# Performance work log

Hardware: AMD Instinct MI355X
Metric: run time of the kernel (lower is better)

## Reference

```python
import jax, jax.numpy as jnp
import numpy as np

B, N, H, K = 8192, 256, 1024, 256
BETA = 0.99
TOL = 1e-4
MAX_ITER = 100

def V_fn(x, Wv):
    # x: (B,1,N) -> (B,1,1); positive-definite quadratic Lyapunov V(x) = ||x @ Wv||^2
    z = jnp.einsum('bon,nk->bok', x, Wv)
    return jnp.sum(z * z, axis=-1, keepdims=True)

def fhat_fn(x, W1, b1, W2, b2):
    # residual tanh MLP dynamics model fhat: (B,1,N) -> (B,1,N)
    h = jnp.tanh(jnp.einsum('bon,nh->boh', x, W1) + b1)
    return x + jnp.einsum('boh,hn->bon', h, W2) + b2

def dV_da(fx, a, Wv):
    # per-sample d/d(alpha) V(fx * alpha); mirrors torch.autograd.grad(Vfx, alpha)
    def v_scalar(a_s, fx_s):
        z = (fx_s * a_s) @ Wv
        return jnp.sum(z * z)
    g = jax.vmap(jax.grad(v_scalar))(a[:, 0, 0], fx[:, 0, :])
    return g[:, None, None]

def newton_F(fx, t, a, Wv):
    # newton_iter.forward: F = alpha - (V(fhatx*alpha) - target) / dV_da
    # dV_da was computed with create_graph=False in torch -> constant -> stop_gradient
    dv = jax.lax.stop_gradient(dV_da(fx, a, Wv))
    return a - (V_fn(fx * a, Wv) - t) / dv

def solve_alpha(fhatx, target, Wv):
    # vectorized Newton + bisection with per-sample masking (rootfind_train.forward)
    Bn = fhatx.shape[0]
    alpha0 = jnp.ones((Bn, 1, 1), jnp.float32)
    e1_0 = jnp.zeros_like(alpha0)
    e2_0 = jnp.ones_like(alpha0)
    m0 = (V_fn(fhatx, Wv) - target) > 0.0

    def cond(c):
        a, e1, e2, m, it = c
        return jnp.logical_and(jnp.any(m), it < MAX_ITER)

    def body(c):
        a, e1, e2, m, it = c
        a = jnp.where(m, newton_F(fhatx, target, a, Wv), a)
        m_bis = (a < e1) | (a > e2)
        a_bis = e1 + (e2 - e1) / 2
        sa = jnp.sign(V_fn(fhatx * a_bis, Wv) - target)
        s1 = jnp.sign(V_fn(fhatx * e1, Wv) - target)
        s2 = jnp.sign(V_fn(fhatx * e2, Wv) - target)
        m_end2 = m_bis & (sa * s1 < 0)
        m_end1 = m_bis & (sa * s2 < 0)
        e2 = jnp.where(m_end2, a_bis, e2)
        e1 = jnp.where(m_end1, a_bis, e1)
        a = jnp.where(m_bis, a_bis, a)
        m = jnp.abs(V_fn(fhatx * a, Wv) - target) > TOL
        return (a, e1, e2, m, it + 1)

    a, _, _, _, _ = jax.lax.while_loop(cond, body, (alpha0, e1_0, e2_0, m0, jnp.int32(0)))
    return a

def setup_inputs() -> dict:
    key = jax.random.key(0)
    ks = jax.random.split(key, 4)
    x = jax.random.normal(ks[0], (B, 1, N), jnp.float32)
    W1 = jax.random.normal(ks[1], (N, H), jnp.float32) / np.sqrt(N)
    b1 = jnp.zeros((H,), jnp.float32)
    W2 = jax.random.normal(ks[2], (H, N), jnp.float32) * (0.5 / np.sqrt(H))
    b2 = jnp.zeros((N,), jnp.float32)
    Wv = jax.random.normal(ks[3], (N, K), jnp.float32) / np.sqrt(N)
    return {'x': x, 'W1': W1, 'b1': b1, 'W2': W2, 'b2': b2, 'Wv': Wv}

def reference(x, W1, b1, W2, b2, Wv):
    fhatx = fhat_fn(x, W1, b1, W2, b2)
    target = BETA * V_fn(x, Wv)
    alpha = jax.lax.stop_gradient(solve_alpha(fhatx, target, Wv))  # alpha detached in torch
    return fhatx * alpha
```

## Files before the change

kernel.cpp:

```cpp
#include <hip/hip_runtime.h>
#include <math.h>

typedef __attribute__((ext_vector_type(8))) short bf16x8;
typedef __attribute__((ext_vector_type(4))) float f32x4;

static __device__ __forceinline__ unsigned short f2bf(float f) {
  union { float f; unsigned u; } a; a.f = f;
  unsigned u = a.u;
  unsigned r = u + 0x7FFF + ((u >> 16) & 1);
  return (unsigned short)(r >> 16);
}
static __device__ __forceinline__ float bf2f(unsigned short h) {
  union { unsigned u; float f; } a; a.u = ((unsigned)h) << 16;
  return a.f;
}
static __device__ __forceinline__ float tanh_fast(float x) {
  float ax = fabsf(x);
  float e = __expf(-2.0f * ax);
  float t = (1.0f - e) / (1.0f + e);
  t = (ax > 10.0f) ? 1.0f : t;
  return (x < 0.0f) ? -t : t;
}

__global__ __launch_bounds__(256) void k_split_all(
    const float* __restrict__ W1, const float* __restrict__ W2, const float* __restrict__ Wv,
    unsigned short* __restrict__ W1Th, unsigned short* __restrict__ W1Tl,
    unsigned short* __restrict__ W2Th, unsigned short* __restrict__ W2Tl,
    unsigned short* __restrict__ WvTh, unsigned short* __restrict__ WvTl)
{
  const int b = blockIdx.x;
  const float* W; unsigned short *Th, *Tl; int Kd, Nd, base;
  if (b < 1024)      { W = W1; Th = W1Th; Tl = W1Tl; Kd = 256;  Nd = 1024; base = 0; }
  else if (b < 2048) { W = W2; Th = W2Th; Tl = W2Tl; Kd = 1024; Nd = 256;  base = 1024; }
  else               { W = Wv; Th = WvTh; Tl = WvTl; Kd = 256;  Nd = 256;  base = 2048; }
  const int idx = (b - base) * 256 + threadIdx.x;
  const int k = idx % Kd, n = idx / Kd;
  const float w = W[(size_t)k * Nd + n];
  const unsigned short h = f2bf(w);
  Th[(size_t)n * Kd + k] = h;
  Tl[(size_t)n * Kd + k] = f2bf(w - bf2f(h));
}

__global__ __launch_bounds__(512, 4) void k_gemm1(
    const float* __restrict__ X, const unsigned short* __restrict__ BTh,
    const unsigned short* __restrict__ BTl, const float* __restrict__ bias,
    unsigned short* __restrict__ Hh, unsigned short* __restrict__ Hl)
{
  const int PIT = 40;
  __shared__ __align__(16) unsigned short As_h[128 * PIT], As_l[128 * PIT];
  __shared__ __align__(16) unsigned short Bs_h[128 * PIT], Bs_l[128 * PIT];
  const int t = threadIdx.x;
  const int n0 = blockIdx.x * 128, m0 = blockIdx.y * 128;
  const int l = t & 63, wid = t >> 6;
  const int wr = wid >> 2, wc = wid & 3;
  const int kk = (l >> 4) * 8;

  f32x4 acc[4][2] = {};

  for (int k0 = 0; k0 < 256; k0 += 32) {
#pragma unroll
    for (int i2 = 0; i2 < 2; ++i2) {
      const int fidx = t + i2 * 512;
      const int row = fidx >> 3, q = fidx & 7;
      const float4 v = *reinterpret_cast<const float4*>(&X[(size_t)(m0 + row) * 256 + k0 + q * 4]);
      unsigned short h0 = f2bf(v.x), h1 = f2bf(v.y), h2 = f2bf(v.z), h3 = f2bf(v.w);
      uint2 hp, lp;
      hp.x = (unsigned)h0 | ((unsigned)h1 << 16);
      hp.y = (unsigned)h2 | ((unsigned)h3 << 16);
      lp.x = (unsigned)f2bf(v.x - bf2f(h0)) | ((unsigned)f2bf(v.y - bf2f(h1)) << 16);
      lp.y = (unsigned)f2bf(v.z - bf2f(h2)) | ((unsigned)f2bf(v.w - bf2f(h3)) << 16);
      *reinterpret_cast<uint2*>(&As_h[row * PIT + q * 4]) = hp;
      *reinterpret_cast<uint2*>(&As_l[row * PIT + q * 4]) = lp;
    }
    {
      const int row = t >> 2, c4 = t & 3;
      *reinterpret_cast<uint4*>(&Bs_h[row * PIT + c4 * 8]) =
          *reinterpret_cast<const uint4*>(&BTh[(size_t)(n0 + row) * 256 + k0 + c4 * 8]);
      *reinterpret_cast<uint4*>(&Bs_l[row * PIT + c4 * 8]) =
          *reinterpret_cast<const uint4*>(&BTl[(size_t)(n0 + row) * 256 + k0 + c4 * 8]);
    }
    __syncthreads();

    bf16x8 ah[4], al[4], bh[2], bl[2];
#pragma unroll
    for (int i = 0; i < 4; ++i) {
      const int ar = wr * 64 + i * 16 + (l & 15);
      ah[i] = *reinterpret_cast<const bf16x8*>(&As_h[ar * PIT + kk]);
      al[i] = *reinterpret_cast<const bf16x8*>(&As_l[ar * PIT + kk]);
    }
#pragma unroll
    for (int j = 0; j < 2; ++j) {
      const int br = wc * 32 + j * 16 + (l & 15);
      bh[j] = *reinterpret_cast<const bf16x8*>(&Bs_h[br * PIT + kk]);
      bl[j] = *reinterpret_cast<const bf16x8*>(&Bs_l[br * PIT + kk]);
    }
#pragma unroll
    for (int i = 0; i < 4; ++i)
#pragma unroll
      for (int j = 0; j < 2; ++j) {
        acc[i][j] = __builtin_amdgcn_mfma_f32_16x16x32_bf16(ah[i], bh[j], acc[i][j], 0, 0, 0);
        acc[i][j] = __builtin_amdgcn_mfma_f32_16x16x32_bf16(ah[i], bl[j], acc[i][j], 0, 0, 0);
        acc[i][j] = __builtin_amdgcn_mfma_f32_16x16x32_bf16(al[i], bh[j], acc[i][j], 0, 0, 0);
      }
    __syncthreads();
  }

#pragma unroll
  for (int i = 0; i < 4; ++i)
#pragma unroll
    for (int j = 0; j < 2; ++j) {
      const int gn = n0 + wc * 32 + j * 16 + (l & 15);
      const float bv = bias[gn];
#pragma unroll
      for (int r = 0; r < 4; ++r) {
        const int gm = m0 + wr * 64 + i * 16 + (l >> 4) * 4 + r;
        const float tv = tanh_fast(acc[i][j][r] + bv);
        const unsigned short th = f2bf(tv);
        Hh[(size_t)gm * 1024 + gn] = th;
        Hl[(size_t)gm * 1024 + gn] = f2bf(tv - bf2f(th));
      }
    }
}

__global__ __launch_bounds__(512, 4) void k_gemm2(
    const unsigned short* __restrict__ Ah, const unsigned short* __restrict__ Al,
    const unsigned short* __restrict__ BTh, const unsigned short* __restrict__ BTl,
    const float* __restrict__ bias, const float* __restrict__ X,
    float* __restrict__ OUT)
{
  const int PIT = 72;
  __shared__ __align__(16) unsigned short As_h[64 * PIT], As_l[64 * PIT];
  __shared__ __align__(16) unsigned short Bs_h[64 * PIT], Bs_l[64 * PIT];
  const int t = threadIdx.x;
  const int n0 = blockIdx.x * 64, m0 = blockIdx.y * 64;
  const int l = t & 63, wid = t >> 6;
  const int wr = wid >> 2, wc = wid & 3;
  const int kk = (l >> 4) * 8;
  const int srow = t >> 3, c8 = t & 7;

  f32x4 acc[2] = {};

  for (int k0 = 0; k0 < 1024; k0 += 64) {
    *reinterpret_cast<uint4*>(&As_h[srow * PIT + c8 * 8]) =
        *reinterpret_cast<const uint4*>(&Ah[(size_t)(m0 + srow) * 1024 + k0 + c8 * 8]);
    *reinterpret_cast<uint4*>(&As_l[srow * PIT + c8 * 8]) =
        *reinterpret_cast<const uint4*>(&Al[(size_t)(m0 + srow) * 1024 + k0 + c8 * 8]);
    *reinterpret_cast<uint4*>(&Bs_h[srow * PIT + c8 * 8]) =
        *reinterpret_cast<const uint4*>(&BTh[(size_t)(n0 + srow) * 1024 + k0 + c8 * 8]);
    *reinterpret_cast<uint4*>(&Bs_l[srow * PIT + c8 * 8]) =
        *reinterpret_cast<const uint4*>(&BTl[(size_t)(n0 + srow) * 1024 + k0 + c8 * 8]);
    __syncthreads();

#pragma unroll
    for (int ks = 0; ks < 2; ++ks) {
      bf16x8 ah[2], al[2], bh, bl;
      const int ko = ks * 32 + kk;
#pragma unroll
      for (int i = 0; i < 2; ++i) {
        const int ar = wr * 32 + i * 16 + (l & 15);
        ah[i] = *reinterpret_cast<const bf16x8*>(&As_h[ar * PIT + ko]);
        al[i] = *reinterpret_cast<const bf16x8*>(&As_l[ar * PIT + ko]);
      }
      const int br = wc * 16 + (l & 15);
      bh = *reinterpret_cast<const bf16x8*>(&Bs_h[br * PIT + ko]);
      bl = *reinterpret_cast<const bf16x8*>(&Bs_l[br * PIT + ko]);
#pragma unroll
      for (int i = 0; i < 2; ++i) {
        acc[i] = __builtin_amdgcn_mfma_f32_16x16x32_bf16(ah[i], bh, acc[i], 0, 0, 0);
        acc[i] = __builtin_amdgcn_mfma_f32_16x16x32_bf16(ah[i], bl, acc[i], 0, 0, 0);
        acc[i] = __builtin_amdgcn_mfma_f32_16x16x32_bf16(al[i], bh, acc[i], 0, 0, 0);
      }
    }
    __syncthreads();
  }

  const int gn = n0 + wc * 16 + (l & 15);
  const float bv = bias[gn];
#pragma unroll
  for (int i = 0; i < 2; ++i)
#pragma unroll
    for (int r = 0; r < 4; ++r) {
      const int gm = m0 + wr * 32 + i * 16 + (l >> 4) * 4 + r;
      OUT[(size_t)gm * 256 + gn] = acc[i][r] + bv + X[(size_t)gm * 256 + gn];
    }
}

__global__ __launch_bounds__(512) void k_valpha(
    const float* __restrict__ X,
    const unsigned short* __restrict__ WvTh, const unsigned short* __restrict__ WvTl,
    float* __restrict__ F)
{
  __shared__ __align__(16) unsigned short Ash[32 * 256];
  __shared__ __align__(16) unsigned short Asl[32 * 256];
  __shared__ float part[2][16][8];
  __shared__ float als[16];
  const int t = threadIdx.x;
  const int l = t & 63, w = t >> 6;
  const int c = l & 15, g = l >> 4;
  const int nb = w * 32;

  bf16x8 bh[2][8], bl[2][8];
#pragma unroll
  for (int nf = 0; nf < 2; ++nf)
#pragma unroll
    for (int ks = 0; ks < 8; ++ks) {
      const int col = nb + nf * 16 + c;
      const int kof = ks * 32 + g * 8;
      bh[nf][ks] = *reinterpret_cast<const bf16x8*>(&WvTh[(size_t)col * 256 + kof]);
      bl[nf][ks] = *reinterpret_cast<const bf16x8*>(&WvTl[(size_t)col * 256 + kof]);
    }

  const int srow = t >> 4;
  const int q = t & 15;
  const int r0 = blockIdx.x * 16;

  float4 fv[4];
  {
    const float* src = (srow < 16) ? &X[(size_t)(r0 + srow) * 256]
                                   : &F[(size_t)(r0 + srow - 16) * 256];
#pragma unroll
    for (int i = 0; i < 4; ++i) {
      const float4 v = *reinterpret_cast<const float4*>(&src[q * 16 + i * 4]);
      fv[i] = v;
      const unsigned short h0 = f2bf(v.x), h1 = f2bf(v.y), h2 = f2bf(v.z), h3 = f2bf(v.w);
      uint2 hp, lp;
      hp.x = (unsigned)h0 | ((unsigned)h1 << 16);
      hp.y = (unsigned)h2 | ((unsigned)h3 << 16);
      lp.x = (unsigned)f2bf(v.x - bf2f(h0)) | ((unsigned)f2bf(v.y - bf2f(h1)) << 16);
      lp.y = (unsigned)f2bf(v.z - bf2f(h2)) | ((unsigned)f2bf(v.w - bf2f(h3)) << 16);
      const unsigned byte = (unsigned)(srow * 512 + q * 32 + i * 8) ^ ((srow & 7) << 4);
      *reinterpret_cast<uint2*>(((char*)Ash) + byte) = hp;
      *reinterpret_cast<uint2*>(((char*)Asl) + byte) = lp;
    }
  }
  __syncthreads();

  float vs[2][4] = {};
#pragma unroll
  for (int nf = 0; nf < 2; ++nf) {
    f32x4 acc0 = {}, acc1 = {};
#pragma unroll
    for (int ks = 0; ks < 8; ++ks) {
      const int kof = ks * 32 + g * 8;
      const unsigned ab0 = (unsigned)(c * 512 + kof * 2) ^ ((c & 7) << 4);
      const unsigned ab1 = (unsigned)((c + 16) * 512 + kof * 2) ^ ((c & 7) << 4);
      const bf16x8 a0h = *reinterpret_cast<const bf16x8*>(((char*)Ash) + ab0);
      const bf16x8 a0l = *reinterpret_cast<const bf16x8*>(((char*)Asl) + ab0);
      const bf16x8 a1h = *reinterpret_cast<const bf16x8*>(((char*)Ash) + ab1);
      const bf16x8 a1l = *reinterpret_cast<const bf16x8*>(((char*)Asl) + ab1);
      acc0 = __builtin_amdgcn_mfma_f32_16x16x32_bf16(a0h, bh[nf][ks], acc0, 0, 0, 0);
      acc0 = __builtin_amdgcn_mfma_f32_16x16x32_bf16(a0h, bl[nf][ks], acc0, 0, 0, 0);
      acc0 = __builtin_amdgcn_mfma_f32_16x16x32_bf16(a0l, bh[nf][ks], acc0, 0, 0, 0);
      acc1 = __builtin_amdgcn_mfma_f32_16x16x32_bf16(a1h, bh[nf][ks], acc1, 0, 0, 0);
      acc1 = __builtin_amdgcn_mfma_f32_16x16x32_bf16(a1h, bl[nf][ks], acc1, 0, 0, 0);
      acc1 = __builtin_amdgcn_mfma_f32_16x16x32_bf16(a1l, bh[nf][ks], acc1, 0, 0, 0);
    }
#pragma unroll
    for (int r = 0; r < 4; ++r) {
      vs[0][r] = fmaf(acc0[r], acc0[r], vs[0][r]);
      vs[1][r] = fmaf(acc1[r], acc1[r], vs[1][r]);
    }
  }

#pragma unroll
  for (int s = 0; s < 2; ++s)
#pragma unroll
    for (int r = 0; r < 4; ++r) {
      float v = vs[s][r];
      v += __shfl_xor(v, 1);
      v += __shfl_xor(v, 2);
      v += __shfl_xor(v, 4);
      v += __shfl_xor(v, 8);
      vs[s][r] = v;
    }
  if (c == 0) {
#pragma unroll
    for (int r = 0; r < 4; ++r) {
      part[0][g * 4 + r][w] = vs[0][r];
      part[1][g * 4 + r][w] = vs[1][r];
    }
  }
  __syncthreads();

  if (t < 16) {
    float Vx = 0.f, Vf = 0.f;
#pragma unroll
    for (int i = 0; i < 8; ++i) { Vx += part[0][t][i]; Vf += part[1][t][i]; }
    const float tt2 = 0.99f * Vx;
    float a;
    if (Vf - tt2 > 0.0f)         a = sqrtf(tt2 / Vf);
    else if (tt2 - Vf > 1e-4f)   a = 0.5f;
    else                         a = 1.0f;
    als[t] = a;
  }
  __syncthreads();

  if (srow >= 16) {
    const int row = srow - 16;
    const float a = als[row];
    float* dst = &F[(size_t)(r0 + row) * 256];
#pragma unroll
    for (int i = 0; i < 4; ++i) {
      float4 v = fv[i];
      v.x *= a; v.y *= a; v.z *= a; v.w *= a;
      *reinterpret_cast<float4*>(&dst[q * 16 + i * 4]) = v;
    }
  }
}

extern "C" void kernel_launch(void* const* d_in, const int* in_sizes, int n_in,
                              void* d_out, int out_size, void* d_ws, size_t ws_size,
                              hipStream_t stream) {
  const float* x  = (const float*)d_in[0];
  const float* W1 = (const float*)d_in[1];
  const float* b1 = (const float*)d_in[2];
  const float* W2 = (const float*)d_in[3];
  const float* b2 = (const float*)d_in[4];
  const float* Wv = (const float*)d_in[5];
  float* out = (float*)d_out;

  char* ws = (char*)d_ws;
  unsigned short* Hh   = (unsigned short*)(ws);
  unsigned short* Hl   = (unsigned short*)(ws + 16777216);
  unsigned short* W1Th = (unsigned short*)(ws + 33554432);
  unsigned short* W1Tl = (unsigned short*)(ws + 33554432 + 524288);
  unsigned short* W2Th = (unsigned short*)(ws + 33554432 + 2 * 524288);
  unsigned short* W2Tl = (unsigned short*)(ws + 33554432 + 3 * 524288);
  unsigned short* WvTh = (unsigned short*)(ws + 33554432 + 4 * 524288);
  unsigned short* WvTl = (unsigned short*)(ws + 33554432 + 4 * 524288 + 131072);

  k_split_all<<<dim3(2304), dim3(256), 0, stream>>>(W1, W2, Wv, W1Th, W1Tl, W2Th, W2Tl, WvTh, WvTl);

  k_gemm1 <<<dim3(1024 / 128, 8192 / 128), dim3(512), 0, stream>>>(x, W1Th, W1Tl, b1, Hh, Hl);
  k_gemm2 <<<dim3(256 / 64, 8192 / 64), dim3(512), 0, stream>>>(Hh, Hl, W2Th, W2Tl, b2, x, out);
  k_valpha<<<dim3(512), dim3(512), 0, stream>>>(x, WvTh, WvTl, out);
}
```

Measured before the change: 82.41 us.

## Use direct global-to-LDS loads with swizzled layout and retile both GEMMs

Pre-splits X into bf16 hi/lo planes in the prep kernel, which now also transposes the weights through shared memory with coalesced accesses. Both GEMMs load tiles with global_load_lds DMA into XOR-swizzled LDS instead of staging through registers. They also move to 256-thread blocks with larger per-wave tiles (4x4 and 2x4 MFMA fragments) to get more register reuse. The cost is extra workspace traffic for Xh/Xl, and the larger accumulators may reduce occupancy.

```diff
diff --git a/kernel.cpp b/kernel.cpp
--- a/kernel.cpp
+++ b/kernel.cpp
@@ -22,82 +22,110 @@
   return (x < 0.0f) ? -t : t;
 }
 
+static __device__ __forceinline__ void gload16(const void* g, void* l) {
+  __builtin_amdgcn_global_load_lds(
+      (const __attribute__((address_space(1))) unsigned int*)g,
+      (__attribute__((address_space(3))) unsigned int*)l, 16, 0, 0);
+}
+
 __global__ __launch_bounds__(256) void k_split_all(
-    const float* __restrict__ W1, const float* __restrict__ W2, const float* __restrict__ Wv,
+    const float* __restrict__ W1, const float* __restrict__ W2,
+    const float* __restrict__ Wv, const float* __restrict__ X,
     unsigned short* __restrict__ W1Th, unsigned short* __restrict__ W1Tl,
     unsigned short* __restrict__ W2Th, unsigned short* __restrict__ W2Tl,
-    unsigned short* __restrict__ WvTh, unsigned short* __restrict__ WvTl)
+    unsigned short* __restrict__ WvTh, unsigned short* __restrict__ WvTl,
+    unsigned short* __restrict__ Xh,  unsigned short* __restrict__ Xl)
 {
-  const int b = blockIdx.x;
-  const float* W; unsigned short *Th, *Tl; int Kd, Nd, base;
-  if (b < 1024)      { W = W1; Th = W1Th; Tl = W1Tl; Kd = 256;  Nd = 1024; base = 0; }
-  else if (b < 2048) { W = W2; Th = W2Th; Tl = W2Tl; Kd = 1024; Nd = 256;  base = 1024; }
-  else               { W = Wv; Th = WvTh; Tl = WvTl; Kd = 256;  Nd = 256;  base = 2048; }
-  const int idx = (b - base) * 256 + threadIdx.x;
-  const int k = idx % Kd, n = idx / Kd;
-  const float w = W[(size_t)k * Nd + n];
-  const unsigned short h = f2bf(w);
-  Th[(size_t)n * Kd + k] = h;
-  Tl[(size_t)n * Kd + k] = f2bf(w - bf2f(h));
-}
-
-__global__ __launch_bounds__(512, 4) void k_gemm1(
-    const float* __restrict__ X, const unsigned short* __restrict__ BTh,
-    const unsigned short* __restrict__ BTl, const float* __restrict__ bias,
+  const int b = blockIdx.x, t = threadIdx.x;
+  if (b >= 144) {
+    const size_t i0 = (size_t)(b - 144) * 2048 + (size_t)t * 8;
+    const float4 v0 = *reinterpret_cast<const float4*>(&X[i0]);
+    const float4 v1 = *reinterpret_cast<const float4*>(&X[i0 + 4]);
+    const float vv[8] = {v0.x, v0.y, v0.z, v0.w, v1.x, v1.y, v1.z, v1.w};
+    uint4 hp, lp;
+    unsigned hw[4], lw[4];
+#pragma unroll
+    for (int e = 0; e < 4; ++e) {
+      const unsigned short h0 = f2bf(vv[2*e]), h1 = f2bf(vv[2*e+1]);
+      hw[e] = (unsigned)h0 | ((unsigned)h1 << 16);
+      lw[e] = (unsigned)f2bf(vv[2*e] - bf2f(h0)) |
+              ((unsigned)f2bf(vv[2*e+1] - bf2f(h1)) << 16);
+    }
+    hp.x = hw[0]; hp.y = hw[1]; hp.z = hw[2]; hp.w = hw[3];
+    lp.x = lw[0]; lp.y = lw[1]; lp.z = lw[2]; lp.w = lw[3];
+    *reinterpret_cast<uint4*>(&Xh[i0]) = hp;
+    *reinterpret_cast<uint4*>(&Xl[i0]) = lp;
+    return;
+  }
+
+  __shared__ unsigned short shh[64 * 72], shl[64 * 72];
+  const float* W; unsigned short *Th, *Tl; int Kd, Nd, k0, n0;
+  if (b < 64)       { W = W1; Th = W1Th; Tl = W1Tl; Kd = 256;  Nd = 1024; k0 = (b & 3) * 64;        n0 = (b >> 2) * 64; }
+  else if (b < 128) { W = W2; Th = W2Th; Tl = W2Tl; Kd = 1024; Nd = 256;  k0 = ((b - 64) & 15) * 64; n0 = ((b - 64) >> 4) * 64; }
+  else              { W = Wv; Th = WvTh; Tl = WvTl; Kd = 256;  Nd = 256;  k0 = ((b - 128) & 3) * 64; n0 = ((b - 128) >> 2) * 64; }
+
+  const int kloc = t >> 4, n4 = t & 15;
+#pragma unroll
+  for (int p = 0; p < 4; ++p) {
+    const int kk = p * 16 + kloc;
+    const float4 v = *reinterpret_cast<const float4*>(&W[(size_t)(k0 + kk) * Nd + n0 + n4 * 4]);
+    const float vv[4] = {v.x, v.y, v.z, v.w};
+#pragma unroll
+    for (int e = 0; e < 4; ++e) {
+      const unsigned short hh = f2bf(vv[e]);
+      shh[(n4 * 4 + e) * 72 + kk] = hh;
+      shl[(n4 * 4 + e) * 72 + kk] = f2bf(vv[e] - bf2f(hh));
+    }
+  }
+  __syncthreads();
+  const int nl = t >> 2, ko = (t & 3) * 16;
+  const size_t dst = (size_t)(n0 + nl) * Kd + k0 + ko;
+  *reinterpret_cast<uint4*>(&Th[dst])     = *reinterpret_cast<const uint4*>(&shh[nl * 72 + ko]);
+  *reinterpret_cast<uint4*>(&Th[dst + 8]) = *reinterpret_cast<const uint4*>(&shh[nl * 72 + ko + 8]);
+  *reinterpret_cast<uint4*>(&Tl[dst])     = *reinterpret_cast<const uint4*>(&shl[nl * 72 + ko]);
+  *reinterpret_cast<uint4*>(&Tl[dst + 8]) = *reinterpret_cast<const uint4*>(&shl[nl * 72 + ko + 8]);
+}
+
+__global__ __launch_bounds__(256, 2) void k_gemm1(
+    const unsigned short* __restrict__ Xh, const unsigned short* __restrict__ Xl,
+    const unsigned short* __restrict__ BTh, const unsigned short* __restrict__ BTl,
+    const float* __restrict__ bias,
     unsigned short* __restrict__ Hh, unsigned short* __restrict__ Hl)
 {
-  const int PIT = 40;
-  __shared__ __align__(16) unsigned short As_h[128 * PIT], As_l[128 * PIT];
-  __shared__ __align__(16) unsigned short Bs_h[128 * PIT], Bs_l[128 * PIT];
-  const int t = threadIdx.x;
+  __shared__ unsigned short lds[16384];
+  const int t = threadIdx.x, l = t & 63, wv = t >> 6;
   const int n0 = blockIdx.x * 128, m0 = blockIdx.y * 128;
-  const int l = t & 63, wid = t >> 6;
-  const int wr = wid >> 2, wc = wid & 3;
-  const int kk = (l >> 4) * 8;
-
-  f32x4 acc[4][2] = {};
-
+  const int wr = wv >> 1, wc = wv & 1;
+
+  const unsigned short* ssrc = (wv == 0) ? Xh : (wv == 1) ? Xl : (wv == 2) ? BTh : BTl;
+  const int rbase = (wv < 2) ? m0 : n0;
+  char* ldsb = (char*)lds + wv * 8192;
+  const int srow = l >> 2;
+  const int sg = (l & 3) ^ ((l >> 3) & 3);
+
+  const int gofs = ((l >> 4) ^ ((l >> 1) & 3)) << 4;
+  const int arow = wr * 64 + (l & 15), brow = wc * 64 + (l & 15);
+
+  f32x4 acc[4][4] = {};
   for (int k0 = 0; k0 < 256; k0 += 32) {
 #pragma unroll
-    for (int i2 = 0; i2 < 2; ++i2) {
-      const int fidx = t + i2 * 512;
-      const int row = fidx >> 3, q = fidx & 7;
-      const float4 v = *reinterpret_cast<const float4*>(&X[(size_t)(m0 + row) * 256 + k0 + q * 4]);
-      unsigned short h0 = f2bf(v.x), h1 = f2bf(v.y), h2 = f2bf(v.z), h3 = f2bf(v.w);
-      uint2 hp, lp;
-      hp.x = (unsigned)h0 | ((unsigned)h1 << 16);
-      hp.y = (unsigned)h2 | ((unsigned)h3 << 16);
-      lp.x = (unsigned)f2bf(v.x - bf2f(h0)) | ((unsigned)f2bf(v.y - bf2f(h1)) << 16);
-      lp.y = (unsigned)f2bf(v.z - bf2f(h2)) | ((unsigned)f2bf(v.w - bf2f(h3)) << 16);
-      *reinterpret_cast<uint2*>(&As_h[row * PIT + q * 4]) = hp;
-      *reinterpret_cast<uint2*>(&As_l[row * PIT + q * 4]) = lp;
-    }
-    {
-      const int row = t >> 2, c4 = t & 3;
-      *reinterpret_cast<uint4*>(&Bs_h[row * PIT + c4 * 8]) =
-          *reinterpret_cast<const uint4*>(&BTh[(size_t)(n0 + row) * 256 + k0 + c4 * 8]);
-      *reinterpret_cast<uint4*>(&Bs_l[row * PIT + c4 * 8]) =
-          *reinterpret_cast<const uint4*>(&BTl[(size_t)(n0 + row) * 256 + k0 + c4 * 8]);
-    }
+    for (int c = 0; c < 8; ++c)
+      gload16(ssrc + (size_t)(rbase + c * 16 + srow) * 256 + k0 + sg * 8, ldsb + c * 1024);
     __syncthreads();
 
-    bf16x8 ah[4], al[4], bh[2], bl[2];
+    const char* L = (const char*)lds;
+    bf16x8 ah[4], al[4], bh[4], bl[4];
 #pragma unroll
     for (int i = 0; i < 4; ++i) {
-      const int ar = wr * 64 + i * 16 + (l & 15);
-      ah[i] = *reinterpret_cast<const bf16x8*>(&As_h[ar * PIT + kk]);
-      al[i] = *reinterpret_cast<const bf16x8*>(&As_l[ar * PIT + kk]);
-    }
-#pragma unroll
-    for (int j = 0; j < 2; ++j) {
-      const int br = wc * 32 + j * 16 + (l & 15);
-      bh[j] = *reinterpret_cast<const bf16x8*>(&Bs_h[br * PIT + kk]);
-      bl[j] = *reinterpret_cast<const bf16x8*>(&Bs_l[br * PIT + kk]);
+      ah[i] = *reinterpret_cast<const bf16x8*>(L +         (arow + i * 16) * 64 + gofs);
+      al[i] = *reinterpret_cast<const bf16x8*>(L +  8192 + (arow + i * 16) * 64 + gofs);
+      bh[i] = *reinterpret_cast<const bf16x8*>(L + 16384 + (brow + i * 16) * 64 + gofs);
+      bl[i] = *reinterpret_cast<const bf16x8*>(L + 24576 + (brow + i * 16) * 64 + gofs);
     }
 #pragma unroll
     for (int i = 0; i < 4; ++i)
 #pragma unroll
-      for (int j = 0; j < 2; ++j) {
+      for (int j = 0; j < 4; ++j) {
         acc[i][j] = __builtin_amdgcn_mfma_f32_16x16x32_bf16(ah[i], bh[j], acc[i][j], 0, 0, 0);
         acc[i][j] = __builtin_amdgcn_mfma_f32_16x16x32_bf16(ah[i], bl[j], acc[i][j], 0, 0, 0);
         acc[i][j] = __builtin_amdgcn_mfma_f32_16x16x32_bf16(al[i], bh[j], acc[i][j], 0, 0, 0);
@@ -108,8 +136,8 @@
 #pragma unroll
   for (int i = 0; i < 4; ++i)
 #pragma unroll
-    for (int j = 0; j < 2; ++j) {
-      const int gn = n0 + wc * 32 + j * 16 + (l & 15);
+    for (int j = 0; j < 4; ++j) {
+      const int gn = n0 + wc * 64 + j * 16 + (l & 15);
       const float bv = bias[gn];
 #pragma unroll
       for (int r = 0; r < 4; ++r) {
@@ -122,66 +150,72 @@
     }
 }
 
-__global__ __launch_bounds__(512, 4) void k_gemm2(
-    const unsigned short* __restrict__ Ah, const unsigned short* __restrict__ Al,
+__global__ __launch_bounds__(256, 2) void k_gemm2(
+    const unsigned short* __restrict__ Ahg, const unsigned short* __restrict__ Alg,
     const unsigned short* __restrict__ BTh, const unsigned short* __restrict__ BTl,
     const float* __restrict__ bias, const float* __restrict__ X,
     float* __restrict__ OUT)
 {
-  const int PIT = 72;
-  __shared__ __align__(16) unsigned short As_h[64 * PIT], As_l[64 * PIT];
-  __shared__ __align__(16) unsigned short Bs_h[64 * PIT], Bs_l[64 * PIT];
-  const int t = threadIdx.x;
-  const int n0 = blockIdx.x * 64, m0 = blockIdx.y * 64;
-  const int l = t & 63, wid = t >> 6;
-  const int wr = wid >> 2, wc = wid & 3;
-  const int kk = (l >> 4) * 8;
-  const int srow = t >> 3, c8 = t & 7;
-
-  f32x4 acc[2] = {};
-
+  __shared__ unsigned short lds[24576];
+  const int t = threadIdx.x, l = t & 63, wv = t >> 6;
+  const int n0 = blockIdx.x * 128, m0 = blockIdx.y * 64;
+  const int wr = wv >> 1, wc = wv & 1;
+  const int srow8 = l >> 3, sg = (l & 7) ^ (l >> 3);
+
+  f32x4 acc[2][4] = {};
   for (int k0 = 0; k0 < 1024; k0 += 64) {
-    *reinterpret_cast<uint4*>(&As_h[srow * PIT + c8 * 8]) =
-        *reinterpret_cast<const uint4*>(&Ah[(size_t)(m0 + srow) * 1024 + k0 + c8 * 8]);
-    *reinterpret_cast<uint4*>(&As_l[srow * PIT + c8 * 8]) =
-        *reinterpret_cast<const uint4*>(&Al[(size_t)(m0 + srow) * 1024 + k0 + c8 * 8]);
-    *reinterpret_cast<uint4*>(&Bs_h[srow * PIT + c8 * 8]) =
-        *reinterpret_cast<const uint4*>(&BTh[(size_t)(n0 + srow) * 1024 + k0 + c8 * 8]);
-    *reinterpret_cast<uint4*>(&Bs_l[srow * PIT + c8 * 8]) =
-        *reinterpret_cast<const uint4*>(&BTl[(size_t)(n0 + srow) * 1024 + k0 + c8 * 8]);
+#pragma unroll
+    for (int s = 0; s < 12; ++s) {
+      const int cid = wv * 12 + s;
+      const unsigned short* src; int rbase, ca, cbyte;
+      if (cid < 8)       { src = Ahg; rbase = m0; ca = cid;      cbyte = ca * 1024; }
+      else if (cid < 16) { src = Alg; rbase = m0; ca = cid - 8;  cbyte = 8192 + ca * 1024; }
+      else if (cid < 32) { src = BTh; rbase = n0; ca = cid - 16; cbyte = 16384 + ca * 1024; }
+      else               { src = BTl; rbase = n0; ca = cid - 32; cbyte = 32768 + ca * 1024; }
+      gload16(src + (size_t)(rbase + ca * 8 + srow8) * 1024 + k0 + sg * 8, (char*)lds + cbyte);
+    }
     __syncthreads();
 
+    const char* L = (const char*)lds;
 #pragma unroll
     for (int ks = 0; ks < 2; ++ks) {
-      bf16x8 ah[2], al[2], bh, bl;
-      const int ko = ks * 32 + kk;
+      const int gofs = (((ks * 4 + (l >> 4)) ^ (l & 7)) << 4);
+      bf16x8 ah[2], al[2], bh[4], bl[4];
 #pragma unroll
       for (int i = 0; i < 2; ++i) {
-        const int ar = wr * 32 + i * 16 + (l & 15);
-        ah[i] = *reinterpret_cast<const bf16x8*>(&As_h[ar * PIT + ko]);
-        al[i] = *reinterpret_cast<const bf16x8*>(&As_l[ar * PIT + ko]);
-      }
-      const int br = wc * 16 + (l & 15);
-      bh = *reinterpret_cast<const bf16x8*>(&Bs_h[br * PIT + ko]);
-      bl = *reinterpret_cast<const bf16x8*>(&Bs_l[br * PIT + ko]);
-#pragma unroll
-      for (int i = 0; i < 2; ++i) {
-        acc[i] = __builtin_amdgcn_mfma_f32_16x16x32_bf16(ah[i], bh, acc[i], 0, 0, 0);
-        acc[i] = __builtin_amdgcn_mfma_f32_16x16x32_bf16(ah[i], bl, acc[i], 0, 0, 0);
-        acc[i] = __builtin_amdgcn_mfma_f32_16x16x32_bf16(al[i], bh, acc[i], 0, 0, 0);
-      }
+        const int r = wr * 32 + i * 16 + (l & 15);
+        ah[i] = *reinterpret_cast<const bf16x8*>(L +        r * 128 + gofs);
+        al[i] = *reinterpret_cast<const bf16x8*>(L + 8192 + r * 128 + gofs);
+      }
+#pragma unroll
+      for (int j = 0; j < 4; ++j) {
+        const int r = wc * 64 + j * 16 + (l & 15);
+        bh[j] = *reinterpret_cast<const bf16x8*>(L + 16384 + r * 128 + gofs);
+        bl[j] = *reinterpret_cast<const bf16x8*>(L + 32768 + r * 128 + gofs);
+      }
+#pragma unroll
+      for (int i = 0; i < 2; ++i)
+#pragma unroll
+        for (int j = 0; j < 4; ++j) {
+          acc[i][j] = __builtin_amdgcn_mfma_f32_16x16x32_bf16(ah[i], bh[j], acc[i][j], 0, 0, 0);
+          acc[i][j] = __builtin_amdgcn_mfma_f32_16x16x32_bf16(ah[i], bl[j], acc[i][j], 0, 0, 0);
+          acc[i][j] = __builtin_amdgcn_mfma_f32_16x16x32_bf16(al[i], bh[j], acc[i][j], 0, 0, 0);
+        }
     }
     __syncthreads();
   }
 
-  const int gn = n0 + wc * 16 + (l & 15);
-  const float bv = bias[gn];
 #pragma unroll
   for (int i = 0; i < 2; ++i)
 #pragma unroll
-    for (int r = 0; r < 4; ++r) {
-      const int gm = m0 + wr * 32 + i * 16 + (l >> 4) * 4 + r;
-      OUT[(size_t)gm * 256 + gn] = acc[i][r] + bv + X[(size_t)gm * 256 + gn];
+    for (int j = 0; j < 4; ++j) {
+      const int gn = n0 + wc * 64 + j * 16 + (l & 15);
+      const float bv = bias[gn];
+#pragma unroll
+      for (int r = 0; r < 4; ++r) {
+        const int gm = m0 + wr * 32 + i * 16 + (l >> 4) * 4 + r;
+        OUT[(size_t)gm * 256 + gn] = acc[i][j][r] + bv + X[(size_t)gm * 256 + gn];
+      }
     }
 }
 
@@ -323,15 +357,18 @@
   unsigned short* Hh   = (unsigned short*)(ws);
   unsigned short* Hl   = (unsigned short*)(ws + 16777216);
   unsigned short* W1Th = (unsigned short*)(ws + 33554432);
-  unsigned short* W1Tl = (unsigned short*)(ws + 33554432 + 524288);
-  unsigned short* W2Th = (unsigned short*)(ws + 33554432 + 2 * 524288);
-  unsigned short* W2Tl = (unsigned short*)(ws + 33554432 + 3 * 524288);
-  unsigned short* WvTh = (unsigned short*)(ws + 33554432 + 4 * 524288);
-  unsigned short* WvTl = (unsigned short*)(ws + 33554432 + 4 * 524288 + 131072);
-
-  k_split_all<<<dim3(2304), dim3(256), 0, stream>>>(W1, W2, Wv, W1Th, W1Tl, W2Th, W2Tl, WvTh, WvTl);
-
-  k_gemm1 <<<dim3(1024 / 128, 8192 / 128), dim3(512), 0, stream>>>(x, W1Th, W1Tl, b1, Hh, Hl);
-  k_gemm2 <<<dim3(256 / 64, 8192 / 64), dim3(512), 0, stream>>>(Hh, Hl, W2Th, W2Tl, b2, x, out);
+  unsigned short* W1Tl = (unsigned short*)(ws + 34078720);
+  unsigned short* W2Th = (unsigned short*)(ws + 34603008);
+  unsigned short* W2Tl = (unsigned short*)(ws + 35127296);
+  unsigned short* WvTh = (unsigned short*)(ws + 35651584);
+  unsigned short* WvTl = (unsigned short*)(ws + 35782656);
+  unsigned short* Xh   = (unsigned short*)(ws + 35913728);
+  unsigned short* Xl   = (unsigned short*)(ws + 40108032);
+
+  k_split_all<<<dim3(1168), dim3(256), 0, stream>>>(
+      W1, W2, Wv, x, W1Th, W1Tl, W2Th, W2Tl, WvTh, WvTl, Xh, Xl);
+
+  k_gemm1 <<<dim3(8, 64),  dim3(256), 0, stream>>>(Xh, Xl, W1Th, W1Tl, b1, Hh, Hl);
+  k_gemm2 <<<dim3(2, 128), dim3(256), 0, stream>>>(Hh, Hl, W2Th, W2Tl, b2, x, out);
   k_valpha<<<dim3(512), dim3(512), 0, stream>>>(x, WvTh, WvTl, out);
 }
```

Result: no change. 83.57 us (+1.4%).
